# Kernel tuning notes

Measured on AMD Instinct MI355X. Metric: run time of the kernel, lower is better.

Reference implementation:

```python
import jax, jax.numpy as jnp
import numpy as np

NUM_EXPERTS = 8
CAP_FACTOR = 1.0
MIN_CAPACITY = 4


def setup_inputs() -> dict:
    key = jax.random.key(0)
    k0, k1, k2, k3 = jax.random.split(key, 4)
    H, F, E = 2048, 8192, NUM_EXPERTS
    hidden_states = jax.random.normal(k0, (4, 2048, H), dtype=jnp.float32)
    wg = jax.random.normal(k1, (H, E), dtype=jnp.float32) * 0.02
    w1 = jax.random.normal(k2, (E, H, F), dtype=jnp.float32) * 0.02
    b1 = jnp.zeros((E, F), dtype=jnp.float32)
    w2 = jax.random.normal(k3, (E, F, H), dtype=jnp.float32) * 0.02
    b2 = jnp.zeros((E, H), dtype=jnp.float32)
    return {"hidden_states": hidden_states, "wg": wg, "w1": w1, "b1": b1,
            "w2": w2, "b2": b2}


def reference(hidden_states, wg, w1, b1, w2, b2):
    E = NUM_EXPERTS
    M = hidden_states.shape[-1]
    x = hidden_states.reshape(-1, M)                     # [S, M] tokens
    S = x.shape[0]
    capacity = max(int(np.ceil(S / E * CAP_FACTOR)), MIN_CAPACITY)  # static

    # --- top-1 gating (DeepSpeed top1gating, fp32) ---
    logits = x.astype(jnp.float32) @ wg                  # [S, E]
    gates = jax.nn.softmax(logits, axis=-1)              # [S, E]
    idx1 = jnp.argmax(gates, axis=1)                     # [S]
    mask1 = jax.nn.one_hot(idx1, E, dtype=jnp.int32)     # [S, E]

    # load-balancing aux loss and per-expert counts
    me = jnp.mean(gates, axis=0)
    ce = jnp.mean(mask1.astype(jnp.float32), axis=0)
    l_aux = jnp.sum(me * ce) * E
    exp_counts = jnp.sum(mask1, axis=0)                  # [E]

    # capacity enforcement (use_rts=False -> keep earliest tokens per expert)
    locations1 = jnp.cumsum(mask1, axis=0) - 1           # [S, E] slot index
    mask1 = mask1 * (locations1 < capacity).astype(jnp.int32)
    mask1f = mask1.astype(gates.dtype)
    gates = gates * mask1f                               # zero dropped/other experts
    locs_s = jnp.sum(locations1 * mask1, axis=1)         # [S] slot of each token
    locs_sc = jax.nn.one_hot(locs_s, capacity, dtype=gates.dtype)  # [S, C]

    # combine / dispatch tensors
    combine = jnp.einsum('se,sc->sec', gates, locs_sc)   # [S, E, C]
    dispatch = (combine > 0).astype(x.dtype)             # bool mask as float

    # dispatch -> grouped expert MLP -> combine
    dispatched = jnp.einsum('sec,sm->ecm', dispatch, x)  # [E, C, M]
    h = jax.nn.gelu(jnp.einsum('ecm,emf->ecf', dispatched, w1) + b1[:, None, :])
    expert_out = jnp.einsum('ecf,efm->ecm', h, w2) + b2[:, None, :]
    out = jnp.einsum('sec,ecm->sm', combine.astype(x.dtype), expert_out)

    return out.reshape(hidden_states.shape), l_aux, exp_counts
```

## Files before the change

kernel.cpp:

```cpp
#include <hip/hip_runtime.h>
#include <stdint.h>

#define E_ 8
#define S_ 8192
#define H_ 2048
#define F_ 8192
#define C_ 1024
#define OUTN (S_*H_)

typedef __bf16 bf16x8 __attribute__((ext_vector_type(8)));
typedef float  f32x4  __attribute__((ext_vector_type(4)));
typedef unsigned short us8 __attribute__((ext_vector_type(8)));

__device__ __forceinline__ unsigned short f2bf(float f) {
    union { float f; unsigned u; } v; v.f = f;
    unsigned r = (v.u + 0x7FFFu + ((v.u >> 16) & 1u)) >> 16;
    return (unsigned short)r;
}

__device__ __forceinline__ void gload16(const void* g, void* l) {
    auto gp = (const __attribute__((address_space(1))) void*)(unsigned long long)(uintptr_t)g;
    auto lp = (__attribute__((address_space(3))) void*)(unsigned int)(uintptr_t)l;
    __builtin_amdgcn_global_load_lds(gp, lp, 16, 0, 0);
}

#define SB() __builtin_amdgcn_sched_barrier(0)
#define BAR() do { SB(); __builtin_amdgcn_s_barrier(); SB(); } while(0)
#define DSR(d, a, o) asm volatile("ds_read_b128 %0, %1 offset:" #o : "=v"(d) : "v"(a))
#define WLGKM(n) do { asm volatile("s_waitcnt lgkmcnt(" #n ")" ::: "memory"); SB(); } while(0)
#define WVM(n)   do { asm volatile("s_waitcnt vmcnt(" #n ")"   ::: "memory"); SB(); } while(0)
#define MM16(accv, af, bf) accv = __builtin_amdgcn_mfma_f32_16x16x32_bf16(af, bf, accv, 0, 0, 0)

__global__ void zero_kernel(float* __restrict__ o, int n) {
    int i = blockIdx.x * blockDim.x + threadIdx.x;
    int st = gridDim.x * blockDim.x;
    for (; i < n; i += st) __builtin_nontemporal_store(0.f, &o[i]);
}

__global__ __launch_bounds__(256)
void transpose_cvt(const float* __restrict__ src, unsigned short* __restrict__ dst,
                   int R, int Cc)
{
    __shared__ float t[64][65];
    int tilesR = R >> 6, tilesC = Cc >> 6;
    int per_e = tilesR * tilesC;
    int bid = blockIdx.x;
    int e  = bid / per_e;
    int rm = bid - e * per_e;
    int tc = rm / tilesR;
    int tr = rm - tc * tilesR;

    const float* s = src + (size_t)e * R * Cc + (size_t)(tr * 64) * Cc + tc * 64;
    int tid = threadIdx.x;
    int rr = tid >> 4;
    int cc = (tid & 15) << 2;
#pragma unroll
    for (int i = 0; i < 4; i++) {
        float4 v = *(const float4*)(s + (size_t)(rr + i * 16) * Cc + cc);
        t[rr + i * 16][cc + 0] = v.x;
        t[rr + i * 16][cc + 1] = v.y;
        t[rr + i * 16][cc + 2] = v.z;
        t[rr + i * 16][cc + 3] = v.w;
    }
    __syncthreads();
    int nl = tid >> 2;
    int kq = (tid & 3) << 4;
    us8 o0, o1;
#pragma unroll
    for (int i = 0; i < 8; i++) o0[i] = f2bf(t[kq + i][nl]);
#pragma unroll
    for (int i = 0; i < 8; i++) o1[i] = f2bf(t[kq + 8 + i][nl]);
    unsigned short* d = dst + (size_t)e * R * Cc + (size_t)(tc * 64 + nl) * R + tr * 64 + kq;
    *reinterpret_cast<us8*>(d)     = o0;
    *reinterpret_cast<us8*>(d + 8) = o1;
}

__global__ __launch_bounds__(256)
void gating_kernel(const float* __restrict__ x, const float* __restrict__ wg,
                   int* __restrict__ expert_id, float* __restrict__ gate_tok,
                   float* __restrict__ gates_all)
{
    int lane = threadIdx.x & 63;
    int wid  = threadIdx.x >> 6;
    int s = blockIdx.x * 4 + wid;
    const float* xs = x + (size_t)s * H_;
    float p[8];
#pragma unroll
    for (int j = 0; j < 8; j++) p[j] = 0.f;
    for (int h = lane; h < H_; h += 64) {
        float xv = xs[h];
        const float4* w4 = (const float4*)(wg + (size_t)h * 8);
        float4 a = w4[0], b = w4[1];
        p[0] += xv * a.x; p[1] += xv * a.y; p[2] += xv * a.z; p[3] += xv * a.w;
        p[4] += xv * b.x; p[5] += xv * b.y; p[6] += xv * b.z; p[7] += xv * b.w;
    }
#pragma unroll
    for (int off = 32; off; off >>= 1) {
#pragma unroll
        for (int j = 0; j < 8; j++) p[j] += __shfl_xor(p[j], off);
    }
    if (lane == 0) {
        float mx = p[0];
#pragma unroll
        for (int j = 1; j < 8; j++) mx = fmaxf(mx, p[j]);
        float ex[8], sum = 0.f;
#pragma unroll
        for (int j = 0; j < 8; j++) { ex[j] = expf(p[j] - mx); sum += ex[j]; }
        float inv = 1.f / sum;
        int am = 0; float best = p[0];
#pragma unroll
        for (int j = 1; j < 8; j++) if (p[j] > best) { best = p[j]; am = j; }
        expert_id[s] = am;
        gate_tok[s]  = expf(best - mx) * inv;
        float* ga = gates_all + (size_t)s * 8;
#pragma unroll
        for (int j = 0; j < 8; j++) ga[j] = ex[j] * inv;
    }
}

__global__ __launch_bounds__(1024)
void scan_kernel(const int* __restrict__ expert_id,
                 const float* __restrict__ gate_tok,
                 const float* __restrict__ gates_all,
                 int* __restrict__ token_slot,
                 float* __restrict__ gate_slot,
                 float* __restrict__ out_tail)
{
    __shared__ unsigned long long wt0[16], wt1[16];
    __shared__ unsigned long long tot0s, tot1s;
    __shared__ float red[1024 * 8];

    int tid = threadIdx.x;
    for (int i = tid; i < E_ * C_; i += 1024) token_slot[i] = -1;

    int ids[8];
#pragma unroll
    for (int j = 0; j < 8; j++) ids[j] = expert_id[tid * 8 + j];

    unsigned long long c0 = 0, c1 = 0;
#pragma unroll
    for (int j = 0; j < 8; j++) {
        int e = ids[j];
        unsigned long long inc = 1ull << ((e & 3) * 16);
        if (e < 4) c0 += inc; else c1 += inc;
    }
    unsigned long long s0 = c0, s1 = c1;
    int lane = tid & 63, w = tid >> 6;
#pragma unroll
    for (int off = 1; off < 64; off <<= 1) {
        unsigned long long t0 = __shfl_up(s0, off);
        unsigned long long t1 = __shfl_up(s1, off);
        if (lane >= off) { s0 += t0; s1 += t1; }
    }
    if (lane == 63) { wt0[w] = s0; wt1[w] = s1; }
    __syncthreads();
    unsigned long long off0 = 0, off1 = 0;
    for (int i = 0; i < w; i++) { off0 += wt0[i]; off1 += wt1[i]; }
    unsigned long long p0 = off0 + s0 - c0;
    unsigned long long p1 = off1 + s1 - c1;

#pragma unroll
    for (int j = 0; j < 8; j++) {
        int stok = tid * 8 + j;
        int e = ids[j];
        int sh = (e & 3) * 16;
        int slot = (int)(((e < 4 ? p0 : p1) >> sh) & 0xFFFFull);
        if (slot < C_) {
            token_slot[e * C_ + slot] = stok;
            gate_slot[e * C_ + slot]  = gate_tok[stok];
        }
        if (e < 4) p0 += 1ull << sh; else p1 += 1ull << sh;
    }
    if (tid == 1023) { tot0s = off0 + s0; tot1s = off1 + s1; }

    float me[8];
#pragma unroll
    for (int e2 = 0; e2 < 8; e2++) me[e2] = 0.f;
#pragma unroll
    for (int j = 0; j < 8; j++) {
        const float* ga = gates_all + (size_t)(tid * 8 + j) * 8;
#pragma unroll
        for (int e2 = 0; e2 < 8; e2++) me[e2] += ga[e2];
    }
#pragma unroll
    for (int e2 = 0; e2 < 8; e2++) red[tid * 8 + e2] = me[e2];
    __syncthreads();
    for (int st = 512; st > 0; st >>= 1) {
        if (tid < st) {
#pragma unroll
            for (int e2 = 0; e2 < 8; e2++) red[tid * 8 + e2] += red[(tid + st) * 8 + e2];
        }
        __syncthreads();
    }
    if (tid == 0) {
        float laux = 0.f;
#pragma unroll
        for (int e2 = 0; e2 < 8; e2++) {
            unsigned long long tv = (e2 < 4) ? tot0s : tot1s;
            float cnt = (float)((tv >> ((e2 & 3) * 16)) & 0xFFFFull);
            laux += red[e2] * cnt;
            out_tail[1 + e2] = cnt;
        }
        out_tail[0] = laux * (8.f / (8192.f * 8192.f));
    }
}

__global__ __launch_bounds__(256)
void gather_kernel(const float* __restrict__ x, const int* __restrict__ token_slot,
                   unsigned short* __restrict__ disp)
{
    int slot = blockIdx.x;
    int tok = token_slot[slot];
    int t = threadIdx.x;
    us8* d = reinterpret_cast<us8*>(disp + (size_t)slot * H_ + t * 8);
    if (tok < 0) {
        us8 z;
#pragma unroll
        for (int i = 0; i < 8; i++) z[i] = 0;
        *d = z;
        return;
    }
    const float4* s4 = (const float4*)(x + (size_t)tok * H_ + t * 8);
    float4 a = s4[0], b = s4[1];
    us8 o;
    o[0] = f2bf(a.x); o[1] = f2bf(a.y); o[2] = f2bf(a.z); o[3] = f2bf(a.w);
    o[4] = f2bf(b.x); o[5] = f2bf(b.y); o[6] = f2bf(b.z); o[7] = f2bf(b.w);
    *d = o;
}

template<int EPI, int K, int N>
__global__ __launch_bounds__(512, 2)
void gemmra(const unsigned short* __restrict__ A,
            const unsigned short* __restrict__ B,
            const float* __restrict__ bias,
            unsigned short* __restrict__ hout,
            float* __restrict__ fout,
            const int* __restrict__ token_slot,
            const float* __restrict__ gate_slot,
            int Mt, int Nt)
{
    __shared__ char lds[131072];
    constexpr int KB  = K * 2;
    constexpr int QG  = 64 * KB;
    constexpr int NTI = K / 64;

    int nwg = gridDim.x;
    int bid = blockIdx.x;
    int cpx = nwg >> 3;
    int wg  = (bid & 7) * cpx + (bid >> 3);
    int per_e = Mt * Nt;
    int e  = wg / per_e;
    int r  = wg - e * per_e;
    int nt = r / Mt;
    int mt = r - nt * Mt;

    int tid  = threadIdx.x;
    int lane = tid & 63;
    int wid  = tid >> 6;
    int wr = wid >> 2, wc = wid & 3;

    const char* Ag = (const char*)(A + ((size_t)e * 1024 + (size_t)mt * 256) * (size_t)K);
    const char* Bg = (const char*)(B + ((size_t)e * N    + (size_t)nt * 256) * (size_t)K);

    int r16s   = (tid >> 2) & 15;
    int scs    = ((tid & 3) * 16) ^ ((r16s & 8) << 2);
    int colblk = (tid >> 6) & 1;
    int rb0    = tid >> 7;
    int off0 = (rb0 * 16 + r16s) * KB + colblk * 64 + scs;
    int widb = wid * 1024;

    int lread = (lane & 15) * 64 + (((lane >> 4) * 16) ^ ((lane & 8) << 2));

    auto SQ = [&](int dstbyte, const char* src) {
        gload16(src + off0, (char*)lds + dstbyte + widb);
    };

#pragma unroll
    for (int j = 0; j < 4; j++) SQ(j * 8192,          Ag + j * QG);
#pragma unroll
    for (int j = 0; j < 4; j++) SQ(65536 + j * 8192,  Bg + j * QG);
#pragma unroll
    for (int j = 0; j < 4; j++) SQ(32768 + j * 8192,  Ag + j * QG + 128);
#pragma unroll
    for (int j = 0; j < 4; j++) SQ(98304 + j * 8192,  Bg + j * QG + 128);
    WVM(8);
    BAR();

    unsigned a0 = (unsigned)(uintptr_t)lds + wr * 16384 + lread;
    unsigned b0 = (unsigned)(uintptr_t)lds + 65536 + (wc >> 1) * 16384 + (wc & 1) * 8192 + lread;

    bf16x8 alo[4][2], ahi[4][2], blo[2][2], bhi[2][2];

    DSR(alo[0][0], a0, 0);    DSR(alo[0][1], a0, 1024);
    DSR(alo[1][0], a0, 2048); DSR(alo[1][1], a0, 3072);
    DSR(alo[2][0], a0, 4096); DSR(alo[2][1], a0, 5120);
    DSR(alo[3][0], a0, 6144); DSR(alo[3][1], a0, 7168);
    DSR(blo[0][0], b0, 0);    DSR(blo[0][1], b0, 1024);
    DSR(blo[1][0], b0, 2048); DSR(blo[1][1], b0, 3072);

    f32x4 acc[8][4];
    f32x4 zv = {0.f, 0.f, 0.f, 0.f};
#pragma unroll
    for (int i = 0; i < 8; i++)
#pragma unroll
        for (int j = 0; j < 4; j++) acc[i][j] = zv;

    for (int t = 0; t < NTI; ++t) {
        int bsel = (t & 1) << 15;
        unsigned av  = a0 + bsel;
        unsigned bv  = b0 + bsel;
        unsigned avn = av ^ 32768;
        unsigned bvn = bv ^ 32768;

        DSR(bhi[0][0], bv, 4096); DSR(bhi[0][1], bv, 5120);
        DSR(bhi[1][0], bv, 6144); DSR(bhi[1][1], bv, 7168);
        WLGKM(4);
        __builtin_amdgcn_s_setprio(1);
#pragma unroll
        for (int mi = 0; mi < 4; mi++)
#pragma unroll
            for (int ni = 0; ni < 2; ni++) {
                MM16(acc[mi][ni], alo[mi][0], blo[ni][0]);
                MM16(acc[mi][ni], alo[mi][1], blo[ni][1]);
            }
        __builtin_amdgcn_s_setprio(0);

        DSR(ahi[0][0], av, 8192);  DSR(ahi[0][1], av, 9216);
        DSR(ahi[1][0], av, 10240); DSR(ahi[1][1], av, 11264);
        DSR(ahi[2][0], av, 12288); DSR(ahi[2][1], av, 13312);
        DSR(ahi[3][0], av, 14336); DSR(ahi[3][1], av, 15360);
        WLGKM(8);
        __builtin_amdgcn_s_setprio(1);
#pragma unroll
        for (int mi = 0; mi < 4; mi++)
#pragma unroll
            for (int ni = 0; ni < 2; ni++) {
                MM16(acc[mi][ni + 2], alo[mi][0], bhi[ni][0]);
                MM16(acc[mi][ni + 2], alo[mi][1], bhi[ni][1]);
            }
        __builtin_amdgcn_s_setprio(0);

        WLGKM(0);
        __builtin_amdgcn_s_setprio(1);
#pragma unroll
        for (int mi = 0; mi < 4; mi++)
#pragma unroll
            for (int ni = 0; ni < 2; ni++) {
                MM16(acc[mi + 4][ni], ahi[mi][0], blo[ni][0]);
                MM16(acc[mi + 4][ni], ahi[mi][1], blo[ni][1]);
            }
        __builtin_amdgcn_s_setprio(0);
        BAR();

        if (t + 2 < NTI) {
            size_t ko = (size_t)(t + 2) * 128;
#pragma unroll
            for (int j = 0; j < 4; j++) SQ(bsel + j * 8192,         Ag + j * QG + ko);
#pragma unroll
            for (int j = 0; j < 4; j++) SQ(bsel + 65536 + j * 8192, Bg + j * QG + ko);
            WVM(8);
        } else {
            WVM(0);
        }
        BAR();
        if (t + 1 < NTI) {
            DSR(alo[0][0], avn, 0);    DSR(alo[0][1], avn, 1024);
            DSR(alo[1][0], avn, 2048); DSR(alo[1][1], avn, 3072);
            DSR(alo[2][0], avn, 4096); DSR(alo[2][1], avn, 5120);
            DSR(alo[3][0], avn, 6144); DSR(alo[3][1], avn, 7168);
            DSR(blo[0][0], bvn, 0);    DSR(blo[0][1], bvn, 1024);
            DSR(blo[1][0], bvn, 2048); DSR(blo[1][1], bvn, 3072);
        }
        __builtin_amdgcn_s_setprio(1);
#pragma unroll
        for (int mi = 0; mi < 4; mi++)
#pragma unroll
            for (int ni = 0; ni < 2; ni++) {
                MM16(acc[mi + 4][ni + 2], ahi[mi][0], bhi[ni][0]);
                MM16(acc[mi + 4][ni + 2], ahi[mi][1], bhi[ni][1]);
            }
        __builtin_amdgcn_s_setprio(0);
    }

    int rbase = wr * 128 + (lane >> 4) * 4;
    int cbase = wc * 64 + (lane & 15);

    if (EPI == 0) {
        size_t rowg = (size_t)e * C_ + (size_t)mt * 256;
        float bb4[4];
#pragma unroll
        for (int ni = 0; ni < 4; ni++)
            bb4[ni] = bias[(size_t)e * N + nt * 256 + cbase + ni * 16];
#pragma unroll
        for (int mi = 0; mi < 8; mi++) {
#pragma unroll
            for (int rr2 = 0; rr2 < 4; rr2++) {
                int m = rbase + mi * 16 + rr2;
                size_t rb = (rowg + (size_t)m) * (size_t)N + nt * 256 + cbase;
#pragma unroll
                for (int ni = 0; ni < 4; ni++) {
                    float v = acc[mi][ni][rr2] + bb4[ni];
                    float u2 = 1.5957691216057308f * (v + 0.044715f * v * v * v);
                    float gl = v * __frcp_rn(1.f + __expf(-u2));
                    hout[rb + ni * 16] = f2bf(gl);
                }
            }
        }
    } else {
        float bb4[4];
#pragma unroll
        for (int ni = 0; ni < 4; ni++)
            bb4[ni] = bias[(size_t)e * N + nt * 256 + cbase + ni * 16];
#pragma unroll
        for (int mi = 0; mi < 8; mi++) {
#pragma unroll
            for (int rr2 = 0; rr2 < 4; rr2++) {
                int c = mt * 256 + rbase + mi * 16 + rr2;
                int tok = token_slot[e * C_ + c];
                if (tok < 0) continue;
                float g = gate_slot[e * C_ + c];
                size_t rb = (size_t)tok * (size_t)N + nt * 256 + cbase;
#pragma unroll
                for (int ni = 0; ni < 4; ni++) {
                    float v = (acc[mi][ni][rr2] + bb4[ni]) * g;
                    __builtin_nontemporal_store(v, &fout[rb + ni * 16]);
                }
            }
        }
    }
}

extern "C" void kernel_launch(void* const* d_in, const int* in_sizes, int n_in,
                              void* d_out, int out_size, void* d_ws, size_t ws_size,
                              hipStream_t stream)
{
    const float* x   = (const float*)d_in[0];
    const float* wgp = (const float*)d_in[1];
    const float* w1  = (const float*)d_in[2];
    const float* b1  = (const float*)d_in[3];
    const float* w2  = (const float*)d_in[4];
    const float* b2  = (const float*)d_in[5];
    float* out = (float*)d_out;

    char* ws = (char*)d_ws;
    unsigned short* w1t  = (unsigned short*)(ws);
    unsigned short* w2t  = (unsigned short*)(ws + 268435456ull);
    unsigned short* disp = (unsigned short*)(ws + 536870912ull);
    unsigned short* hbuf = (unsigned short*)(ws + 570425344ull);
    int*   expert_id  = (int*)  (ws + 704643072ull);
    float* gate_tok   = (float*)(ws + 704675840ull);
    float* gates_all  = (float*)(ws + 704708608ull);
    int*   token_slot = (int*)  (ws + 704970752ull);
    float* gate_slot  = (float*)(ws + 705003520ull);

    zero_kernel<<<4096, 256, 0, stream>>>(out, out_size);
    transpose_cvt<<<8 * 128 * 32, 256, 0, stream>>>(w2, w2t, 8192, 2048);
    transpose_cvt<<<8 * 32 * 128, 256, 0, stream>>>(w1, w1t, 2048, 8192);
    gating_kernel<<<2048, 256, 0, stream>>>(x, wgp, expert_id, gate_tok, gates_all);
    scan_kernel<<<1, 1024, 0, stream>>>(expert_id, gate_tok, gates_all, token_slot, gate_slot, out + OUTN);
    gather_kernel<<<8192, 256, 0, stream>>>(x, token_slot, disp);
    gemmra<0, 2048, 8192><<<1024, 512, 0, stream>>>(disp, w1t, b1, hbuf, nullptr, nullptr, nullptr, 4, 32);
    gemmra<1, 8192, 2048><<<256, 512, 0, stream>>>(hbuf, w2t, b2, nullptr, out, token_slot, gate_slot, 4, 8);
}
```

Before: 888.8 us.

## Restructure grouped GEMM mainloop into four-stage 32-wide K pipeline with new swizzle

Rewrites the expert GEMM main loop to stage K in 32-element slices across four LDS buffers, with two slices in flight, instead of double-buffered 64-element slices. It adopts a new XOR swizzle for the 64-byte rows and a simpler MFMA schedule where each slice feeds a single K-step of MFMAs. The goal is to overlap global-to-LDS loads with compute more deeply and to cut LDS bank conflicts. In exchange it adds a full wait and barrier at every pair of slices, and the per-slice loads are smaller.

```diff
diff --git a/kernel.cpp b/kernel.cpp
--- a/kernel.cpp
+++ b/kernel.cpp
@@ -230,7 +230,7 @@
 
 template<int EPI, int K, int N>
 __global__ __launch_bounds__(512, 2)
-void gemmra(const unsigned short* __restrict__ A,
+void gemmfr(const unsigned short* __restrict__ A,
             const unsigned short* __restrict__ B,
             const float* __restrict__ bias,
             unsigned short* __restrict__ hout,
@@ -240,9 +240,8 @@
             int Mt, int Nt)
 {
     __shared__ char lds[131072];
-    constexpr int KB  = K * 2;
-    constexpr int QG  = 64 * KB;
-    constexpr int NTI = K / 64;
+    constexpr int PB  = K * 2;
+    constexpr int NTI = K / 32;
 
     int nwg = gridDim.x;
     int bid = blockIdx.x;
@@ -262,41 +261,31 @@
     const char* Ag = (const char*)(A + ((size_t)e * 1024 + (size_t)mt * 256) * (size_t)K);
     const char* Bg = (const char*)(B + ((size_t)e * N    + (size_t)nt * 256) * (size_t)K);
 
-    int r16s   = (tid >> 2) & 15;
-    int scs    = ((tid & 3) * 16) ^ ((r16s & 8) << 2);
-    int colblk = (tid >> 6) & 1;
-    int rb0    = tid >> 7;
-    int off0 = (rb0 * 16 + r16s) * KB + colblk * 64 + scs;
+    int r_t = wid * 16 + (lane >> 2);
+    int sx  = (lane & 3) ^ ((r_t >> 1) & 3);
+    size_t off0 = (size_t)r_t * PB + (size_t)sx * 16;
+    size_t off1 = off0 + (size_t)128 * PB;
     int widb = wid * 1024;
 
-    int lread = (lane & 15) * 64 + (((lane >> 4) * 16) ^ ((lane & 8) << 2));
-
-    auto SQ = [&](int dstbyte, const char* src) {
-        gload16(src + off0, (char*)lds + dstbyte + widb);
+    auto STAGE = [&](int u) {
+        int bb = (u & 3) * 32768;
+        const char* Au = Ag + (size_t)u * 64;
+        const char* Bu = Bg + (size_t)u * 64;
+        gload16(Au + off0, (char*)lds + bb + widb);
+        gload16(Au + off1, (char*)lds + bb + 8192 + widb);
+        gload16(Bu + off0, (char*)lds + bb + 16384 + widb);
+        gload16(Bu + off1, (char*)lds + bb + 24576 + widb);
     };
 
-#pragma unroll
-    for (int j = 0; j < 4; j++) SQ(j * 8192,          Ag + j * QG);
-#pragma unroll
-    for (int j = 0; j < 4; j++) SQ(65536 + j * 8192,  Bg + j * QG);
-#pragma unroll
-    for (int j = 0; j < 4; j++) SQ(32768 + j * 8192,  Ag + j * QG + 128);
-#pragma unroll
-    for (int j = 0; j < 4; j++) SQ(98304 + j * 8192,  Bg + j * QG + 128);
-    WVM(8);
-    BAR();
-
-    unsigned a0 = (unsigned)(uintptr_t)lds + wr * 16384 + lread;
-    unsigned b0 = (unsigned)(uintptr_t)lds + 65536 + (wc >> 1) * 16384 + (wc & 1) * 8192 + lread;
-
-    bf16x8 alo[4][2], ahi[4][2], blo[2][2], bhi[2][2];
-
-    DSR(alo[0][0], a0, 0);    DSR(alo[0][1], a0, 1024);
-    DSR(alo[1][0], a0, 2048); DSR(alo[1][1], a0, 3072);
-    DSR(alo[2][0], a0, 4096); DSR(alo[2][1], a0, 5120);
-    DSR(alo[3][0], a0, 6144); DSR(alo[3][1], a0, 7168);
-    DSR(blo[0][0], b0, 0);    DSR(blo[0][1], b0, 1024);
-    DSR(blo[1][0], b0, 2048); DSR(blo[1][1], b0, 3072);
+    int r0A = wr * 128 + (lane & 15);
+    int xA  = (((lane >> 4) ^ ((r0A >> 1) & 3))) * 16;
+    int r0B = wc * 64 + (lane & 15);
+    int xB  = (((lane >> 4) ^ ((r0B >> 1) & 3))) * 16;
+    unsigned baseA = (unsigned)(uintptr_t)lds + r0A * 64 + xA;
+    unsigned baseB = (unsigned)(uintptr_t)lds + 16384 + r0B * 64 + xB;
+
+    STAGE(0);
+    STAGE(1);
 
     f32x4 acc[8][4];
     f32x4 zv = {0.f, 0.f, 0.f, 0.f};
@@ -305,80 +294,60 @@
 #pragma unroll
         for (int j = 0; j < 4; j++) acc[i][j] = zv;
 
-    for (int t = 0; t < NTI; ++t) {
-        int bsel = (t & 1) << 15;
-        unsigned av  = a0 + bsel;
-        unsigned bv  = b0 + bsel;
-        unsigned avn = av ^ 32768;
-        unsigned bvn = bv ^ 32768;
-
-        DSR(bhi[0][0], bv, 4096); DSR(bhi[0][1], bv, 5120);
-        DSR(bhi[1][0], bv, 6144); DSR(bhi[1][1], bv, 7168);
+    bf16x8 xalo[4], xb[4], yalo[4], yb[4], h[4];
+
+    for (int t = 0; t < NTI; t += 2) {
+        int bufX = ((t >> 1) & 1) * 65536;
+        unsigned aX = baseA + bufX, bX = baseB + bufX;
+        unsigned aY = aX + 32768,   bY = bX + 32768;
+
+        WLGKM(0);
+        WVM(0);
+        BAR();
+        if (t + 2 < NTI) STAGE(t + 2);
+        if (t + 3 < NTI) STAGE(t + 3);
+
+        DSR(xalo[0], aX, 0);    DSR(xalo[1], aX, 1024);
+        DSR(xalo[2], aX, 2048); DSR(xalo[3], aX, 3072);
+        DSR(xb[0], bX, 0);      DSR(xb[1], bX, 1024);
+        DSR(xb[2], bX, 2048);   DSR(xb[3], bX, 3072);
+
+        DSR(h[0], aX, 4096); DSR(h[1], aX, 5120);
+        DSR(h[2], aX, 6144); DSR(h[3], aX, 7168);
         WLGKM(4);
         __builtin_amdgcn_s_setprio(1);
 #pragma unroll
         for (int mi = 0; mi < 4; mi++)
 #pragma unroll
-            for (int ni = 0; ni < 2; ni++) {
-                MM16(acc[mi][ni], alo[mi][0], blo[ni][0]);
-                MM16(acc[mi][ni], alo[mi][1], blo[ni][1]);
-            }
+            for (int ni = 0; ni < 4; ni++) MM16(acc[mi][ni], xalo[mi], xb[ni]);
         __builtin_amdgcn_s_setprio(0);
-
-        DSR(ahi[0][0], av, 8192);  DSR(ahi[0][1], av, 9216);
-        DSR(ahi[1][0], av, 10240); DSR(ahi[1][1], av, 11264);
-        DSR(ahi[2][0], av, 12288); DSR(ahi[2][1], av, 13312);
-        DSR(ahi[3][0], av, 14336); DSR(ahi[3][1], av, 15360);
-        WLGKM(8);
+        WLGKM(0);
+        DSR(yalo[0], aY, 0);    DSR(yalo[1], aY, 1024);
+        DSR(yalo[2], aY, 2048); DSR(yalo[3], aY, 3072);
+        DSR(yb[0], bY, 0);      DSR(yb[1], bY, 1024);
+        DSR(yb[2], bY, 2048);   DSR(yb[3], bY, 3072);
         __builtin_amdgcn_s_setprio(1);
 #pragma unroll
         for (int mi = 0; mi < 4; mi++)
 #pragma unroll
-            for (int ni = 0; ni < 2; ni++) {
-                MM16(acc[mi][ni + 2], alo[mi][0], bhi[ni][0]);
-                MM16(acc[mi][ni + 2], alo[mi][1], bhi[ni][1]);
-            }
+            for (int ni = 0; ni < 4; ni++) MM16(acc[mi + 4][ni], h[mi], xb[ni]);
         __builtin_amdgcn_s_setprio(0);
 
+        DSR(h[0], aY, 4096); DSR(h[1], aY, 5120);
+        DSR(h[2], aY, 6144); DSR(h[3], aY, 7168);
+        WLGKM(4);
+        __builtin_amdgcn_s_setprio(1);
+#pragma unroll
+        for (int mi = 0; mi < 4; mi++)
+#pragma unroll
+            for (int ni = 0; ni < 4; ni++) MM16(acc[mi][ni], yalo[mi], yb[ni]);
+        __builtin_amdgcn_s_setprio(0);
         WLGKM(0);
         __builtin_amdgcn_s_setprio(1);
 #pragma unroll
         for (int mi = 0; mi < 4; mi++)
 #pragma unroll
-            for (int ni = 0; ni < 2; ni++) {
-                MM16(acc[mi + 4][ni], ahi[mi][0], blo[ni][0]);
-                MM16(acc[mi + 4][ni], ahi[mi][1], blo[ni][1]);
-            }
-        __builtin_amdgcn_s_setprio(0);
-        BAR();
-
-        if (t + 2 < NTI) {
-            size_t ko = (size_t)(t + 2) * 128;
-#pragma unroll
-            for (int j = 0; j < 4; j++) SQ(bsel + j * 8192,         Ag + j * QG + ko);
-#pragma unroll
-            for (int j = 0; j < 4; j++) SQ(bsel + 65536 + j * 8192, Bg + j * QG + ko);
-            WVM(8);
-        } else {
-            WVM(0);
-        }
-        BAR();
-        if (t + 1 < NTI) {
-            DSR(alo[0][0], avn, 0);    DSR(alo[0][1], avn, 1024);
-            DSR(alo[1][0], avn, 2048); DSR(alo[1][1], avn, 3072);
-            DSR(alo[2][0], avn, 4096); DSR(alo[2][1], avn, 5120);
-            DSR(alo[3][0], avn, 6144); DSR(alo[3][1], avn, 7168);
-            DSR(blo[0][0], bvn, 0);    DSR(blo[0][1], bvn, 1024);
-            DSR(blo[1][0], bvn, 2048); DSR(blo[1][1], bvn, 3072);
-        }
-        __builtin_amdgcn_s_setprio(1);
-#pragma unroll
-        for (int mi = 0; mi < 4; mi++)
-#pragma unroll
-            for (int ni = 0; ni < 2; ni++) {
-                MM16(acc[mi + 4][ni + 2], ahi[mi][0], bhi[ni][0]);
-                MM16(acc[mi + 4][ni + 2], ahi[mi][1], bhi[ni][1]);
-            }
+            for (int ni = 0; ni < 4; ni++) MM16(acc[mi + 4][ni], h[mi], yb[ni]);
         __builtin_amdgcn_s_setprio(0);
     }
 
@@ -459,6 +428,6 @@
     gating_kernel<<<2048, 256, 0, stream>>>(x, wgp, expert_id, gate_tok, gates_all);
     scan_kernel<<<1, 1024, 0, stream>>>(expert_id, gate_tok, gates_all, token_slot, gate_slot, out + OUTN);
     gather_kernel<<<8192, 256, 0, stream>>>(x, token_slot, disp);
-    gemmra<0, 2048, 8192><<<1024, 512, 0, stream>>>(disp, w1t, b1, hbuf, nullptr, nullptr, nullptr, 4, 32);
-    gemmra<1, 8192, 2048><<<256, 512, 0, stream>>>(hbuf, w2t, b2, nullptr, out, token_slot, gate_slot, 4, 8);
-}
+    gemmfr<0, 2048, 8192><<<1024, 512, 0, stream>>>(disp, w1t, b1, hbuf, nullptr, nullptr, nullptr, 4, 32);
+    gemmfr<1, 8192, 2048><<<256, 512, 0, stream>>>(hbuf, w2t, b2, nullptr, out, token_slot, gate_slot, 4, 8);
+}
```

Result: slower. 931.1 us (+4.8%).
